# Performance work log

Measured on AMD Instinct MI355X. Metric: run time of the kernel, lower is better.

The kernel has to match this reference:

```python
import jax, jax.numpy as jnp
import numpy as np

N = 100000      # total nodes
E = 1600000     # total edges
B = 256         # graphs in batch
D_IN = 64       # node_in_dim
D_EMB = 128     # node_emb_dim
D_G = 128       # graph_emb_dim
L = 3           # gnn_layers
H1, H2 = 32, 8  # decoder MLP hidden dims
EPS_LN = 1e-5


def layernorm(h, g, b):
    mu = jnp.mean(h, -1, keepdims=True)
    var = jnp.mean((h - mu) ** 2, -1, keepdims=True)
    return (h - mu) * jax.lax.rsqrt(var + EPS_LN) * g + b


def setup_inputs() -> dict:
    key = jax.random.key(0)
    ks = jax.random.split(key, 16)
    gi = D_IN + D_EMB  # skip-conn GNN input dim

    def w(k, shape, fan):
        return jax.random.normal(k, shape, jnp.float32) / np.sqrt(fan).astype(np.float32)

    return {
        "x": jax.random.normal(ks[0], (N, D_IN), jnp.float32),
        "edge_index": jax.random.randint(ks[1], (2, E), 0, N),
        "batch_indices": jnp.sort(jax.random.randint(ks[2], (N,), 0, B)),
        "W_in": w(ks[3], (D_IN, D_EMB), D_IN), "b_in": jnp.zeros((D_EMB,), jnp.float32),
        "eps": jnp.zeros((L,), jnp.float32),  # GINConv train_eps init 0
        "mlp_W1": w(ks[4], (L, gi, D_EMB), gi), "mlp_b1": jnp.zeros((L, D_EMB), jnp.float32),
        "mlp_W2": w(ks[5], (L, D_EMB, D_EMB), D_EMB), "mlp_b2": jnp.zeros((L, D_EMB), jnp.float32),
        "ln_g": jnp.ones((L, D_EMB), jnp.float32), "ln_b": jnp.zeros((L, D_EMB), jnp.float32),
        "out_W": w(ks[6], (D_EMB, D_EMB), D_EMB), "out_b": jnp.zeros((D_EMB,), jnp.float32),
        "lnf_g": jnp.ones((D_EMB,), jnp.float32), "lnf_b": jnp.zeros((D_EMB,), jnp.float32),
        "graph_W": w(ks[7], (D_EMB, D_G), D_EMB), "graph_b": jnp.zeros((D_G,), jnp.float32),
        "gln_g": jnp.ones((D_G,), jnp.float32), "gln_b": jnp.zeros((D_G,), jnp.float32),
        "dW1": w(ks[8], (D_IN + D_EMB, H1), D_IN + D_EMB), "db1": jnp.zeros((H1,), jnp.float32),
        "dW2": w(ks[9], (H1, H2), H1), "db2": jnp.zeros((H2,), jnp.float32),
        "dW3": w(ks[10], (H2, 1), H2), "db3": jnp.zeros((1,), jnp.float32),
        "gW1": w(ks[11], (D_G, H1), D_G), "gb1": jnp.zeros((H1,), jnp.float32),
        "gW2": w(ks[12], (H1, H2), H1), "gb2": jnp.zeros((H2,), jnp.float32),
        "gW3": w(ks[13], (H2, 1), H2), "gb3": jnp.zeros((1,), jnp.float32),
    }


def reference(x, edge_index, batch_indices, W_in, b_in, eps, mlp_W1, mlp_b1, mlp_W2, mlp_b2,
              ln_g, ln_b, out_W, out_b, lnf_g, lnf_b, graph_W, graph_b, gln_g, gln_b,
              dW1, db1, dW2, db2, dW3, db3, gW1, gb1, gW2, gb2, gW3, gb3):
    src, dst = edge_index[0], edge_index[1]
    # Encoder: node_in_fc
    h = jax.nn.relu(x @ W_in + b_in)
    for l in range(L):
        gin = jnp.concatenate([x, h], -1)  # skip_conn: [N, D_IN+D_EMB]
        # GIN message passing: sum-aggregate neighbor features at target nodes
        agg = jax.ops.segment_sum(gin[src], dst, num_segments=N)
        z = (1.0 + eps[l]) * gin + agg
        z = jax.nn.relu(z @ mlp_W1[l] + mlp_b1[l]) @ mlp_W2[l] + mlp_b2[l]
        h = jax.nn.elu(layernorm(z, ln_g[l], ln_b[l]))
    # graph embedding: per-node fc+LN then global mean pool over batch segments
    ge = layernorm(jax.nn.relu(h @ graph_W + graph_b), gln_g, gln_b)
    sums = jax.ops.segment_sum(ge, batch_indices, num_segments=B)
    cnt = jax.ops.segment_sum(jnp.ones((N,), ge.dtype), batch_indices, num_segments=B)
    graph_emb = sums / jnp.maximum(cnt, 1.0)[:, None]
    # node_out_fc + final LN
    node_emb = layernorm(jax.nn.relu(h @ out_W + out_b), lnf_g, lnf_b)
    # Decoder: nodewise MLP on [x, node_emb] (skip_conn)
    ni = jnp.concatenate([x, node_emb], -1)
    no = jax.nn.relu(ni @ dW1 + db1)
    no = (jax.nn.relu(no @ dW2 + db2) @ dW3 + db3)[:, 0]  # [N]
    # graphwise residual MLP
    go = jax.nn.relu(graph_emb @ gW1 + gb1)
    go = (jax.nn.relu(go @ gW2 + gb2) @ gW3 + gb3)[:, 0]  # [B]
    return jnp.concatenate([no, go], -1)  # [N+B]
```

## Files before the change

kernel.cpp:

```cpp
#include <hip/hip_runtime.h>
#include <hip/hip_bf16.h>

#define D_IN 64
#define D_EMB 128
#define GI 192
#define H1 32
#define H2 8

typedef __attribute__((ext_vector_type(8))) short bf16x8;
typedef __attribute__((ext_vector_type(4))) float f32x4;

__device__ __forceinline__ unsigned short f2bf(float f) {
    unsigned int u = __float_as_uint(f);
    return (unsigned short)((u + 0x7fffu + ((u >> 16) & 1u)) >> 16);
}
__device__ __forceinline__ float bflo(unsigned int u) { return __uint_as_float(u << 16); }
__device__ __forceinline__ float bfhi(unsigned int u) { return __uint_as_float(u & 0xffff0000u); }
__device__ __forceinline__ unsigned int pk2(unsigned short a, unsigned short b) {
    return (unsigned int)a | ((unsigned int)b << 16);
}

__global__ __launch_bounds__(256) void hist_part_k(const int* __restrict__ dst, int* __restrict__ cnt,
                                                   int E, int N8) {
    int p = blockIdx.x & 7;
    int base = (blockIdx.x >> 3) * 1024;
    int lo = p * N8, hi = lo + N8;
    #pragma unroll
    for (int t = 0; t < 4; ++t) {
        int e = base + t * 256 + threadIdx.x;
        if (e < E) {
            int d = dst[e];
            if (d >= lo && d < hi) atomicAdd(&cnt[d], 1);
        }
    }
}

__global__ __launch_bounds__(256) void scan1_k(const int* __restrict__ cnt, int* __restrict__ loc,
                                               int* __restrict__ bsum, int N) {
    __shared__ int s[256];
    int tid = threadIdx.x;
    int i = blockIdx.x * 256 + tid;
    int v = (i < N) ? cnt[i] : 0;
    s[tid] = v;
    __syncthreads();
    #pragma unroll
    for (int off = 1; off < 256; off <<= 1) {
        int u = (tid >= off) ? s[tid - off] : 0;
        __syncthreads();
        s[tid] += u;
        __syncthreads();
    }
    int incl = s[tid];
    if (i < N) loc[i] = incl - v;
    if (tid == 255) bsum[blockIdx.x] = incl;
}

__global__ __launch_bounds__(512) void scan2_k(int* __restrict__ bsum, int NB) {
    __shared__ int s[512];
    int tid = threadIdx.x;
    int v = (tid < NB) ? bsum[tid] : 0;
    s[tid] = v;
    __syncthreads();
    #pragma unroll
    for (int off = 1; off < 512; off <<= 1) {
        int u = (tid >= off) ? s[tid - off] : 0;
        __syncthreads();
        s[tid] += u;
        __syncthreads();
    }
    if (tid < NB) bsum[tid] = s[tid] - v;
}

__global__ __launch_bounds__(256) void scan3_k(int* __restrict__ rp, const int* __restrict__ bsum,
                                               int* __restrict__ cursor, int N, int E) {
    int i = blockIdx.x * 256 + threadIdx.x;
    if (i < N) {
        int r = rp[i] + bsum[i >> 8];
        rp[i] = r;
        cursor[i] = r;
    } else if (i == N) {
        rp[N] = E;
    }
}

__global__ __launch_bounds__(256) void scatter_part_k(const int* __restrict__ src, const int* __restrict__ dst,
                                                      int* __restrict__ cursor, int* __restrict__ csr,
                                                      int E, int N8) {
    int p = blockIdx.x & 7;
    int base = (blockIdx.x >> 3) * 1024;
    int lo = p * N8, hi = lo + N8;
    #pragma unroll
    for (int t = 0; t < 4; ++t) {
        int e = base + t * 256 + threadIdx.x;
        if (e < E) {
            int d = dst[e];
            if (d >= lo && d < hi) {
                int s = src[e];
                int pos = atomicAdd(&cursor[d], 1);
                csr[pos] = s;
            }
        }
    }
}

__global__ __launch_bounds__(256) void xcvt_k(const float* __restrict__ x, unsigned short* __restrict__ xb,
                                              int total4) {
    int i = blockIdx.x * 256 + threadIdx.x;
    if (i < total4) {
        float4 v = ((const float4*)x)[i];
        ((uint2*)xb)[i] = make_uint2(pk2(f2bf(v.x), f2bf(v.y)), pk2(f2bf(v.z), f2bf(v.w)));
    }
}

__global__ __launch_bounds__(256) void wfrag_all_k(
    const float* __restrict__ W_in, const float* __restrict__ mlp_W1, const float* __restrict__ mlp_W2,
    const float* __restrict__ graph_W, const float* __restrict__ out_W,
    unsigned short* __restrict__ wf_in, unsigned short* __restrict__ wf_w1,
    unsigned short* __restrict__ wf_w2, unsigned short* __restrict__ wf_graph,
    unsigned short* __restrict__ wf_out) {
    int idx = blockIdx.x * 256 + threadIdx.x;
    const float* src;
    unsigned short* dst;
    int local;
    if (idx < 8192) { src = W_in; dst = wf_in; local = idx; }
    else if (idx < 81920) { int t = idx - 8192; int l = t / 24576; local = t - l * 24576;
                            src = mlp_W1 + (size_t)l * 24576; dst = wf_w1 + (size_t)l * 24576; }
    else if (idx < 131072) { int t = idx - 81920; int l = t / 16384; local = t - l * 16384;
                             src = mlp_W2 + (size_t)l * 16384; dst = wf_w2 + (size_t)l * 16384; }
    else if (idx < 147456) { local = idx - 131072; src = graph_W; dst = wf_graph; }
    else { local = idx - 147456; src = out_W; dst = wf_out; }
    int k = local >> 7, c = local & 127;
    dst[(((size_t)(k >> 3) * 128) + c) * 8 + (k & 7)] = f2bf(src[local]);
}

__global__ __launch_bounds__(256) void agg64b_k(const unsigned short* __restrict__ xb,
                                                const int* __restrict__ rp, const int* __restrict__ cs,
                                                unsigned short* __restrict__ outb, int N) {
    int n = blockIdx.x * 8 + (threadIdx.x >> 5);
    int lane = threadIdx.x & 31;
    if (n >= N) return;
    int bg = rp[n], e = rp[n + 1];
    const unsigned int* x2 = (const unsigned int*)xb;
    float sx = 0.f, sy = 0.f;
    int j = bg;
    for (; j + 3 < e; j += 4) {
        unsigned int v0 = x2[(size_t)cs[j] * 32 + lane];
        unsigned int v1 = x2[(size_t)cs[j + 1] * 32 + lane];
        unsigned int v2 = x2[(size_t)cs[j + 2] * 32 + lane];
        unsigned int v3 = x2[(size_t)cs[j + 3] * 32 + lane];
        sx += bflo(v0) + bflo(v1) + bflo(v2) + bflo(v3);
        sy += bfhi(v0) + bfhi(v1) + bfhi(v2) + bfhi(v3);
    }
    for (; j < e; ++j) {
        unsigned int v = x2[(size_t)cs[j] * 32 + lane];
        sx += bflo(v);
        sy += bfhi(v);
    }
    ((unsigned int*)outb)[(size_t)n * 32 + lane] = pk2(f2bf(sx), f2bf(sy));
}

__global__ __launch_bounds__(256) void zxcvt_k(const unsigned short* __restrict__ xb,
                                               const unsigned short* __restrict__ aggxb,
                                               const float* __restrict__ eps,
                                               unsigned short* __restrict__ zx0,
                                               unsigned short* __restrict__ zx1,
                                               unsigned short* __restrict__ zx2, int total2) {
    int i = blockIdx.x * 256 + threadIdx.x;
    if (i >= total2) return;
    unsigned int xv = ((const unsigned int*)xb)[i];
    unsigned int av = ((const unsigned int*)aggxb)[i];
    float xl = bflo(xv), xh = bfhi(xv), al = bflo(av), ah = bfhi(av);
    float e0 = 1.0f + eps[0], e1 = 1.0f + eps[1], e2 = 1.0f + eps[2];
    ((unsigned int*)zx0)[i] = pk2(f2bf(fmaf(e0, xl, al)), f2bf(fmaf(e0, xh, ah)));
    ((unsigned int*)zx1)[i] = pk2(f2bf(fmaf(e1, xl, al)), f2bf(fmaf(e1, xh, ah)));
    ((unsigned int*)zx2)[i] = pk2(f2bf(fmaf(e2, xl, al)), f2bf(fmaf(e2, xh, ah)));
}

__global__ __launch_bounds__(256) void aggz_k(const unsigned short* __restrict__ hb,
                                              const int* __restrict__ rp, const int* __restrict__ cs,
                                              const float* __restrict__ epsp,
                                              unsigned short* __restrict__ zh, int N) {
    int w = threadIdx.x >> 6, lane = threadIdx.x & 63;
    int n = blockIdx.x * 4 + w;
    if (n >= N) return;
    float es = 1.0f + epsp[0];
    int bg = rp[n], e = rp[n + 1];
    const unsigned int* h2 = (const unsigned int*)hb;
    float sx = 0.f, sy = 0.f;
    int j = bg;
    for (; j + 3 < e; j += 4) {
        unsigned int v0 = h2[(size_t)cs[j] * 64 + lane];
        unsigned int v1 = h2[(size_t)cs[j + 1] * 64 + lane];
        unsigned int v2 = h2[(size_t)cs[j + 2] * 64 + lane];
        unsigned int v3 = h2[(size_t)cs[j + 3] * 64 + lane];
        sx += bflo(v0) + bflo(v1) + bflo(v2) + bflo(v3);
        sy += bfhi(v0) + bfhi(v1) + bfhi(v2) + bfhi(v3);
    }
    for (; j < e; ++j) {
        unsigned int v = h2[(size_t)cs[j] * 64 + lane];
        sx += bflo(v);
        sy += bfhi(v);
    }
    unsigned int hv = h2[(size_t)n * 64 + lane];
    sx = fmaf(es, bflo(hv), sx);
    sy = fmaf(es, bfhi(hv), sy);
    ((unsigned int*)zh)[(size_t)n * 64 + lane] = pk2(f2bf(sx), f2bf(sy));
}

template <int RELU, int ELU>
__device__ __forceinline__ void ln_epilogue(
    f32x4 (&acc)[4][4], const float* __restrict__ bias,
    const float* __restrict__ g, const float* __restrict__ b,
    unsigned short* __restrict__ out,
    int rowBase, int wr, int wc, int lg, int l15, int wh,
    float* rsum, float* rsq, int N) {
    float bv[4], gv[4], bbv[4];
    #pragma unroll
    for (int cb = 0; cb < 4; ++cb) {
        int col = wc + cb * 16 + l15;
        bv[cb] = bias[col];
        gv[cb] = g[col];
        bbv[cb] = b[col];
    }
    float ps[4][4], pq[4][4];
    #pragma unroll
    for (int rb = 0; rb < 4; ++rb)
        #pragma unroll
        for (int q = 0; q < 4; ++q) {
            float s = 0.f, sq = 0.f;
            #pragma unroll
            for (int cb = 0; cb < 4; ++cb) {
                float v = acc[rb][cb][q] + bv[cb];
                if (RELU) v = fmaxf(v, 0.f);
                s += v;
                sq += v * v;
            }
            ps[rb][q] = s;
            pq[rb][q] = sq;
        }
    #pragma unroll
    for (int m = 1; m < 16; m <<= 1) {
        #pragma unroll
        for (int rb = 0; rb < 4; ++rb)
            #pragma unroll
            for (int q = 0; q < 4; ++q) {
                ps[rb][q] += __shfl_xor(ps[rb][q], m, 64);
                pq[rb][q] += __shfl_xor(pq[rb][q], m, 64);
            }
    }
    if (l15 == 0) {
        #pragma unroll
        for (int rb = 0; rb < 4; ++rb)
            #pragma unroll
            for (int q = 0; q < 4; ++q) {
                int row = wr + rb * 16 + lg * 4 + q;
                rsum[wh * 128 + row] = ps[rb][q];
                rsq[wh * 128 + row] = pq[rb][q];
            }
    }
    __syncthreads();
    #pragma unroll
    for (int rb = 0; rb < 4; ++rb)
        #pragma unroll
        for (int q = 0; q < 4; ++q) {
            int row = wr + rb * 16 + lg * 4 + q;
            float st = rsum[row] + rsum[128 + row];
            float sqt = rsq[row] + rsq[128 + row];
            float mu = st * (1.f / 128.f);
            float var = sqt * (1.f / 128.f) - mu * mu;
            float rs = rsqrtf(var + 1e-5f);
            int grow = rowBase + row;
            if (grow < N) {
                #pragma unroll
                for (int cb = 0; cb < 4; ++cb) {
                    float v = acc[rb][cb][q] + bv[cb];
                    if (RELU) v = fmaxf(v, 0.f);
                    float y = (v - mu) * rs * gv[cb] + bbv[cb];
                    if (ELU) y = y > 0.f ? y : expm1f(y);
                    out[(size_t)grow * D_EMB + wc + cb * 16 + l15] = f2bf(y);
                }
            }
        }
}

__global__ __launch_bounds__(256) void enc_gemm_k(
    const unsigned short* __restrict__ Abf, const unsigned short* __restrict__ Wf,
    const float* __restrict__ bias, unsigned short* __restrict__ C, int N) {
    const int tid = threadIdx.x;
    const int wid = tid >> 6, lane = tid & 63;
    const int l15 = lane & 15, lg = lane >> 4;
    const int rowBase = blockIdx.x * 128;
    const int wr = (wid >> 1) * 64, wc = (wid & 1) * 64;
    f32x4 zero = {0.f, 0.f, 0.f, 0.f};
    f32x4 acc[4][4];
    #pragma unroll
    for (int i = 0; i < 4; ++i)
        #pragma unroll
        for (int j = 0; j < 4; ++j) acc[i][j] = zero;
    const unsigned short* ap[4];
    #pragma unroll
    for (int rb = 0; rb < 4; ++rb)
        ap[rb] = Abf + (size_t)min(rowBase + wr + rb * 16 + l15, N - 1) * D_IN;

    for (int k0 = 0; k0 < D_IN; k0 += 32) {
        const int G = (k0 >> 3) + lg;
        bf16x8 bfr[4];
        #pragma unroll
        for (int cb = 0; cb < 4; ++cb)
            bfr[cb] = *(const bf16x8*)&Wf[(((size_t)G * 128) + wc + cb * 16 + l15) * 8];
        #pragma unroll
        for (int rb = 0; rb < 4; ++rb) {
            bf16x8 afr = *(const bf16x8*)(ap[rb] + G * 8);
            #pragma unroll
            for (int cb = 0; cb < 4; ++cb)
                acc[rb][cb] = __builtin_amdgcn_mfma_f32_16x16x32_bf16(afr, bfr[cb], acc[rb][cb], 0, 0, 0);
        }
    }
    #pragma unroll
    for (int cb = 0; cb < 4; ++cb) {
        int col = wc + cb * 16 + l15;
        float bvv = bias[col];
        #pragma unroll
        for (int rb = 0; rb < 4; ++rb)
            #pragma unroll
            for (int q = 0; q < 4; ++q) {
                int row = rowBase + wr + rb * 16 + lg * 4 + q;
                if (row < N) C[(size_t)row * D_EMB + col] = f2bf(fmaxf(acc[rb][cb][q] + bvv, 0.f));
            }
    }
}

__global__ __launch_bounds__(256) void gin_layer_k(
    const unsigned short* __restrict__ zxl, const unsigned short* __restrict__ zhb,
    const unsigned short* __restrict__ W1f, const float* __restrict__ b1,
    const unsigned short* __restrict__ W2f, const float* __restrict__ b2,
    const float* __restrict__ lng, const float* __restrict__ lnb,
    unsigned short* __restrict__ hbo, int N) {
    __shared__ unsigned short T1[8 * 128 * 8];
    __shared__ float rsum[2 * 128];
    __shared__ float rsq[2 * 128];

    const int tid = threadIdx.x;
    const int wid = tid >> 6, lane = tid & 63;
    const int l15 = lane & 15, lg = lane >> 4;
    const int rowBase = blockIdx.x * 128;
    const int wr = (wid >> 1) * 64, wc = (wid & 1) * 64;
    const int wh = wid & 1;

    f32x4 zero = {0.f, 0.f, 0.f, 0.f};
    f32x4 acc[4][4];
    #pragma unroll
    for (int i = 0; i < 4; ++i)
        #pragma unroll
        for (int j = 0; j < 4; ++j) acc[i][j] = zero;

    const unsigned short* axp[4];
    const unsigned short* ahp[4];
    #pragma unroll
    for (int rb = 0; rb < 4; ++rb) {
        int ar = min(rowBase + wr + rb * 16 + l15, N - 1);
        axp[rb] = zxl + (size_t)ar * D_IN;
        ahp[rb] = zhb + (size_t)ar * D_EMB;
    }

    for (int k0 = 0; k0 < D_IN; k0 += 32) {
        const int G = (k0 >> 3) + lg;
        bf16x8 bfr[4];
        #pragma unroll
        for (int cb = 0; cb < 4; ++cb)
            bfr[cb] = *(const bf16x8*)&W1f[(((size_t)G * 128) + wc + cb * 16 + l15) * 8];
        #pragma unroll
        for (int rb = 0; rb < 4; ++rb) {
            bf16x8 afr = *(const bf16x8*)(axp[rb] + G * 8);
            #pragma unroll
            for (int cb = 0; cb < 4; ++cb)
                acc[rb][cb] = __builtin_amdgcn_mfma_f32_16x16x32_bf16(afr, bfr[cb], acc[rb][cb], 0, 0, 0);
        }
    }
    for (int k0 = D_IN; k0 < GI; k0 += 32) {
        const int G = (k0 >> 3) + lg;
        const int ZG = ((k0 - D_IN) >> 3) + lg;
        bf16x8 bfr[4];
        #pragma unroll
        for (int cb = 0; cb < 4; ++cb)
            bfr[cb] = *(const bf16x8*)&W1f[(((size_t)G * 128) + wc + cb * 16 + l15) * 8];
        #pragma unroll
        for (int rb = 0; rb < 4; ++rb) {
            bf16x8 afr = *(const bf16x8*)(ahp[rb] + ZG * 8);
            #pragma unroll
            for (int cb = 0; cb < 4; ++cb)
                acc[rb][cb] = __builtin_amdgcn_mfma_f32_16x16x32_bf16(afr, bfr[cb], acc[rb][cb], 0, 0, 0);
        }
    }

    f32x4 acc2[4][4];
    #pragma unroll
    for (int i = 0; i < 4; ++i)
        #pragma unroll
        for (int j = 0; j < 4; ++j) acc2[i][j] = zero;

    #pragma unroll
    for (int c = 0; c < 2; ++c) {
        if (c) __syncthreads();
        if (wc == c * 64) {
            #pragma unroll
            for (int cb = 0; cb < 4; ++cb) {
                int col = wc + cb * 16 + l15;
                int tcol = col - c * 64;
                float bvv = b1[col];
                #pragma unroll
                for (int rb = 0; rb < 4; ++rb)
                    #pragma unroll
                    for (int q = 0; q < 4; ++q) {
                        int row = wr + rb * 16 + lg * 4 + q;
                        float v = fmaxf(acc[rb][cb][q] + bvv, 0.f);
                        T1[(((size_t)(tcol >> 3) * 128) + row) * 8 + (tcol & 7)] = f2bf(v);
                    }
            }
        }
        __syncthreads();
        for (int k0 = c * 64; k0 < c * 64 + 64; k0 += 32) {
            const int G = (k0 >> 3) + lg;
            const int TG = G - c * 8;
            bf16x8 bfr[4];
            #pragma unroll
            for (int cb = 0; cb < 4; ++cb)
                bfr[cb] = *(const bf16x8*)&W2f[(((size_t)G * 128) + wc + cb * 16 + l15) * 8];
            #pragma unroll
            for (int rb = 0; rb < 4; ++rb) {
                bf16x8 afr = *(const bf16x8*)&T1[(((size_t)TG * 128) + wr + rb * 16 + l15) * 8];
                #pragma unroll
                for (int cb = 0; cb < 4; ++cb)
                    acc2[rb][cb] = __builtin_amdgcn_mfma_f32_16x16x32_bf16(afr, bfr[cb], acc2[rb][cb], 0, 0, 0);
            }
        }
    }

    ln_epilogue<0, 1>(acc2, b2, lng, lnb, hbo, rowBase, wr, wc, lg, l15, wh, rsum, rsq, N);
}

__global__ __launch_bounds__(256) void fc2_k(
    const unsigned short* __restrict__ Abf,
    const unsigned short* __restrict__ WfG, const float* __restrict__ biasG,
    const float* __restrict__ gG, const float* __restrict__ bG, unsigned short* __restrict__ outG,
    const unsigned short* __restrict__ WfN, const float* __restrict__ biasN,
    const float* __restrict__ gN, const float* __restrict__ bN, unsigned short* __restrict__ outN,
    int N) {
    __shared__ float rsum[2 * 128];
    __shared__ float rsq[2 * 128];
    const int tid = threadIdx.x;
    const int wid = tid >> 6, lane = tid & 63;
    const int l15 = lane & 15, lg = lane >> 4;
    const int rowBase = blockIdx.x * 128;
    const int wr = (wid >> 1) * 64, wc = (wid & 1) * 64;
    const int wh = wid & 1;
    f32x4 zero = {0.f, 0.f, 0.f, 0.f};
    f32x4 accG[4][4], accN[4][4];
    #pragma unroll
    for (int i = 0; i < 4; ++i)
        #pragma unroll
        for (int j = 0; j < 4; ++j) { accG[i][j] = zero; accN[i][j] = zero; }
    const unsigned short* ap[4];
    #pragma unroll
    for (int rb = 0; rb < 4; ++rb)
        ap[rb] = Abf + (size_t)min(rowBase + wr + rb * 16 + l15, N - 1) * D_EMB;

    for (int k0 = 0; k0 < D_EMB; k0 += 32) {
        const int G = (k0 >> 3) + lg;
        bf16x8 bfrG[4], bfrN[4];
        #pragma unroll
        for (int cb = 0; cb < 4; ++cb) {
            bfrG[cb] = *(const bf16x8*)&WfG[(((size_t)G * 128) + wc + cb * 16 + l15) * 8];
            bfrN[cb] = *(const bf16x8*)&WfN[(((size_t)G * 128) + wc + cb * 16 + l15) * 8];
        }
        #pragma unroll
        for (int rb = 0; rb < 4; ++rb) {
            bf16x8 afr = *(const bf16x8*)(ap[rb] + G * 8);
            #pragma unroll
            for (int cb = 0; cb < 4; ++cb) {
                accG[rb][cb] = __builtin_amdgcn_mfma_f32_16x16x32_bf16(afr, bfrG[cb], accG[rb][cb], 0, 0, 0);
                accN[rb][cb] = __builtin_amdgcn_mfma_f32_16x16x32_bf16(afr, bfrN[cb], accN[rb][cb], 0, 0, 0);
            }
        }
    }
    ln_epilogue<1, 0>(accG, biasG, gG, bG, outG, rowBase, wr, wc, lg, l15, wh, rsum, rsq, N);
    __syncthreads();
    ln_epilogue<1, 0>(accN, biasN, gN, bN, outN, rowBase, wr, wc, lg, l15, wh, rsum, rsq, N);
}

__global__ __launch_bounds__(256) void bounds_k(const int* __restrict__ batch, int* __restrict__ bounds,
                                                int N, int B) {
    int i = blockIdx.x * 256 + threadIdx.x;
    if (i <= B) {
        int lo = 0, hi = N;
        while (lo < hi) { int m = (lo + hi) >> 1; if (batch[m] < i) lo = m + 1; else hi = m; }
        bounds[i] = lo;
    }
}

__global__ __launch_bounds__(128) void pool_part_k(const unsigned short* __restrict__ ge,
                                                   const int* __restrict__ bounds,
                                                   float* __restrict__ gemb) {
    int b = blockIdx.x >> 3;
    int s = blockIdx.x & 7;
    int start = bounds[b], end = bounds[b + 1];
    int len = end - start;
    int c0 = start + (int)(((long long)len * s) >> 3);
    int c1 = start + (int)(((long long)len * (s + 1)) >> 3);
    if (c1 <= c0) return;
    int col = threadIdx.x;
    float sum = 0.f;
    for (int n = c0; n < c1; ++n)
        sum += __uint_as_float((unsigned int)ge[(size_t)n * D_EMB + col] << 16);
    atomicAdd(&gemb[(size_t)b * D_EMB + col], sum);
}

__global__ __launch_bounds__(256) void node_dec_k(
    const float* __restrict__ x, const unsigned short* __restrict__ ne,
    const float* __restrict__ W1, const float* __restrict__ b1,
    const float* __restrict__ W2, const float* __restrict__ b2,
    const float* __restrict__ W3, const float* __restrict__ b3,
    float* __restrict__ out, int N) {
    __shared__ float W1s[GI * H1];
    __shared__ float W2s[H1 * H2];
    __shared__ float W3s[H2];
    __shared__ float b1s[H1], b2s[H2];
    for (int i = threadIdx.x; i < GI * H1; i += 256) W1s[i] = W1[i];
    if (threadIdx.x < H1 * H2) W2s[threadIdx.x] = W2[threadIdx.x];
    if (threadIdx.x < H2) { W3s[threadIdx.x] = W3[threadIdx.x]; b2s[threadIdx.x] = b2[threadIdx.x]; }
    if (threadIdx.x < H1) b1s[threadIdx.x] = b1[threadIdx.x];
    __syncthreads();
    int n = blockIdx.x * 256 + threadIdx.x;
    if (n >= N) return;
    float acc[H1];
    #pragma unroll
    for (int j = 0; j < H1; ++j) acc[j] = b1s[j];
    const float4* xr = (const float4*)(x + (size_t)n * D_IN);
    #pragma unroll 4
    for (int q = 0; q < D_IN / 4; ++q) {
        float4 v = xr[q];
        int k = q * 4;
        #pragma unroll
        for (int j = 0; j < H1; ++j) acc[j] = fmaf(v.x, W1s[(k + 0) * H1 + j], acc[j]);
        #pragma unroll
        for (int j = 0; j < H1; ++j) acc[j] = fmaf(v.y, W1s[(k + 1) * H1 + j], acc[j]);
        #pragma unroll
        for (int j = 0; j < H1; ++j) acc[j] = fmaf(v.z, W1s[(k + 2) * H1 + j], acc[j]);
        #pragma unroll
        for (int j = 0; j < H1; ++j) acc[j] = fmaf(v.w, W1s[(k + 3) * H1 + j], acc[j]);
    }
    const uint4* nr = (const uint4*)(ne + (size_t)n * D_EMB);
    #pragma unroll 4
    for (int q = 0; q < 16; ++q) {
        uint4 v = nr[q];
        float f[8] = {bflo(v.x), bfhi(v.x), bflo(v.y), bfhi(v.y),
                      bflo(v.z), bfhi(v.z), bflo(v.w), bfhi(v.w)};
        int k = D_IN + q * 8;
        #pragma unroll
        for (int e = 0; e < 8; ++e) {
            #pragma unroll
            for (int j = 0; j < H1; ++j) acc[j] = fmaf(f[e], W1s[(k + e) * H1 + j], acc[j]);
        }
    }
    #pragma unroll
    for (int j = 0; j < H1; ++j) acc[j] = fmaxf(acc[j], 0.f);
    float a2[H2];
    #pragma unroll
    for (int m = 0; m < H2; ++m) a2[m] = b2s[m];
    #pragma unroll
    for (int j = 0; j < H1; ++j)
        #pragma unroll
        for (int m = 0; m < H2; ++m) a2[m] = fmaf(acc[j], W2s[j * H2 + m], a2[m]);
    float o = b3[0];
    #pragma unroll
    for (int m = 0; m < H2; ++m) o = fmaf(fmaxf(a2[m], 0.f), W3s[m], o);
    out[n] = o;
}

__global__ __launch_bounds__(256) void graph_dec_k(
    const float* __restrict__ gemb, const int* __restrict__ bounds,
    const float* __restrict__ W1, const float* __restrict__ b1,
    const float* __restrict__ W2, const float* __restrict__ b2,
    const float* __restrict__ W3, const float* __restrict__ b3,
    float* __restrict__ out, int B) {
    __shared__ float W1s[D_EMB * H1];
    __shared__ float W2s[H1 * H2];
    __shared__ float W3s[H2];
    __shared__ float b1s[H1], b2s[H2];
    for (int i = threadIdx.x; i < D_EMB * H1; i += 256) W1s[i] = W1[i];
    if (threadIdx.x < H1 * H2) W2s[threadIdx.x] = W2[threadIdx.x];
    if (threadIdx.x < H2) { W3s[threadIdx.x] = W3[threadIdx.x]; b2s[threadIdx.x] = b2[threadIdx.x]; }
    if (threadIdx.x < H1) b1s[threadIdx.x] = b1[threadIdx.x];
    __syncthreads();
    int gidx = threadIdx.x;
    if (gidx >= B) return;
    int len = bounds[gidx + 1] - bounds[gidx];
    float inv = 1.f / fmaxf((float)len, 1.f);
    float acc[H1];
    #pragma unroll
    for (int j = 0; j < H1; ++j) acc[j] = b1s[j];
    const float4* gr = (const float4*)(gemb + (size_t)gidx * D_EMB);
    for (int q = 0; q < D_EMB / 4; ++q) {
        float4 v = gr[q];
        v.x *= inv; v.y *= inv; v.z *= inv; v.w *= inv;
        int k = q * 4;
        #pragma unroll
        for (int j = 0; j < H1; ++j) acc[j] = fmaf(v.x, W1s[(k + 0) * H1 + j], acc[j]);
        #pragma unroll
        for (int j = 0; j < H1; ++j) acc[j] = fmaf(v.y, W1s[(k + 1) * H1 + j], acc[j]);
        #pragma unroll
        for (int j = 0; j < H1; ++j) acc[j] = fmaf(v.z, W1s[(k + 2) * H1 + j], acc[j]);
        #pragma unroll
        for (int j = 0; j < H1; ++j) acc[j] = fmaf(v.w, W1s[(k + 3) * H1 + j], acc[j]);
    }
    #pragma unroll
    for (int j = 0; j < H1; ++j) acc[j] = fmaxf(acc[j], 0.f);
    float a2[H2];
    #pragma unroll
    for (int m = 0; m < H2; ++m) a2[m] = b2s[m];
    #pragma unroll
    for (int j = 0; j < H1; ++j)
        #pragma unroll
        for (int m = 0; m < H2; ++m) a2[m] = fmaf(acc[j], W2s[j * H2 + m], a2[m]);
    float o = b3[0];
    #pragma unroll
    for (int m = 0; m < H2; ++m) o = fmaf(fmaxf(a2[m], 0.f), W3s[m], o);
    out[gidx] = o;
}

extern "C" void kernel_launch(void* const* d_in, const int* in_sizes, int n_in,
                              void* d_out, int out_size, void* d_ws, size_t ws_size,
                              hipStream_t stream) {
    const float* x       = (const float*)d_in[0];
    const int*   ei      = (const int*)d_in[1];
    const int*   batch   = (const int*)d_in[2];
    const float* W_in    = (const float*)d_in[3];
    const float* b_in    = (const float*)d_in[4];
    const float* eps     = (const float*)d_in[5];
    const float* mlp_W1  = (const float*)d_in[6];
    const float* mlp_b1  = (const float*)d_in[7];
    const float* mlp_W2  = (const float*)d_in[8];
    const float* mlp_b2  = (const float*)d_in[9];
    const float* ln_g    = (const float*)d_in[10];
    const float* ln_b    = (const float*)d_in[11];
    const float* out_W   = (const float*)d_in[12];
    const float* out_b   = (const float*)d_in[13];
    const float* lnf_g   = (const float*)d_in[14];
    const float* lnf_b   = (const float*)d_in[15];
    const float* graph_W = (const float*)d_in[16];
    const float* graph_b = (const float*)d_in[17];
    const float* gln_g   = (const float*)d_in[18];
    const float* gln_b   = (const float*)d_in[19];
    const float* dW1     = (const float*)d_in[20];
    const float* db1     = (const float*)d_in[21];
    const float* dW2     = (const float*)d_in[22];
    const float* db2     = (const float*)d_in[23];
    const float* dW3     = (const float*)d_in[24];
    const float* db3     = (const float*)d_in[25];
    const float* gW1     = (const float*)d_in[26];
    const float* gb1     = (const float*)d_in[27];
    const float* gW2     = (const float*)d_in[28];
    const float* gb2     = (const float*)d_in[29];
    const float* gW3     = (const float*)d_in[30];
    const float* gb3     = (const float*)d_in[31];
    float* out = (float*)d_out;

    const int N = in_sizes[0] / D_IN;
    const int E = in_sizes[1] / 2;
    const int B = out_size - N;
    const int N8 = (N + 7) / 8;

    const int* esrc = ei;
    const int* edst = ei + E;

    size_t off = 0;
    auto alloc = [&](size_t bytes) { size_t o = off; off += (bytes + 255) & ~(size_t)255; return o; };
    char* ws = (char*)d_ws;
    unsigned short* xb    = (unsigned short*)(ws + alloc((size_t)N * D_IN * 2));
    unsigned short* hb0   = (unsigned short*)(ws + alloc((size_t)N * D_EMB * 2));
    unsigned short* hb1   = (unsigned short*)(ws + alloc((size_t)N * D_EMB * 2));
    unsigned short* zh    = (unsigned short*)(ws + alloc((size_t)N * D_EMB * 2));
    unsigned short* aggxb = (unsigned short*)(ws + alloc((size_t)N * D_IN * 2));
    unsigned short* zx0   = (unsigned short*)(ws + alloc((size_t)N * D_IN * 2));
    unsigned short* zx1   = (unsigned short*)(ws + alloc((size_t)N * D_IN * 2));
    unsigned short* zx2   = (unsigned short*)(ws + alloc((size_t)N * D_IN * 2));
    float* gemb = (float*)(ws + alloc((size_t)B * D_EMB * 4));
    unsigned short* wfpool = (unsigned short*)(ws + alloc((size_t)163840 * 2));
    int* row_ptr = (int*)(ws + alloc((size_t)(N + 1) * 4));
    int* cnt     = (int*)(ws + alloc((size_t)N * 4));
    int* bsum    = (int*)(ws + alloc(512 * 4));
    int* bounds  = (int*)(ws + alloc((size_t)(B + 1) * 4));
    int* csr     = (int*)(ws + alloc((size_t)E * 4));
    (void)ws_size;

    unsigned short* wf_in    = wfpool;
    unsigned short* wf_w1    = wf_in + (size_t)64 * 128;
    unsigned short* wf_w2    = wf_w1 + (size_t)3 * 192 * 128;
    unsigned short* wf_graph = wf_w2 + (size_t)3 * 128 * 128;
    unsigned short* wf_out   = wf_graph + (size_t)128 * 128;

    unsigned short* zxs[3] = {zx0, zx1, zx2};

    const int NB = (N + 255) / 256;
    const int gridEP = 8 * ((E + 1023) / 1024);
    const int gridN4 = (N + 3) / 4;
    const int gridG = (N + 127) / 128;

    hipMemsetAsync(cnt, 0, (size_t)N * 4, stream);
    hist_part_k<<<gridEP, 256, 0, stream>>>(edst, cnt, E, N8);
    scan1_k<<<NB, 256, 0, stream>>>(cnt, row_ptr, bsum, N);
    scan2_k<<<1, 512, 0, stream>>>(bsum, NB);
    scan3_k<<<(N + 256) / 256, 256, 0, stream>>>(row_ptr, bsum, cnt, N, E);
    scatter_part_k<<<gridEP, 256, 0, stream>>>(esrc, edst, cnt, csr, E, N8);

    xcvt_k<<<(N * D_IN / 4 + 255) / 256, 256, 0, stream>>>(x, xb, N * D_IN / 4);
    wfrag_all_k<<<640, 256, 0, stream>>>(W_in, mlp_W1, mlp_W2, graph_W, out_W,
                                         wf_in, wf_w1, wf_w2, wf_graph, wf_out);
    bounds_k<<<(B + 256) / 256, 256, 0, stream>>>(batch, bounds, N, B);
    hipMemsetAsync(gemb, 0, (size_t)B * D_EMB * 4, stream);

    agg64b_k<<<(N + 7) / 8, 256, 0, stream>>>(xb, row_ptr, csr, aggxb, N);
    zxcvt_k<<<(N * 32 + 255) / 256, 256, 0, stream>>>(xb, aggxb, eps, zx0, zx1, zx2, N * 32);

    enc_gemm_k<<<gridG, 256, 0, stream>>>(xb, wf_in, b_in, hb0, N);

    unsigned short* hin = hb0;
    unsigned short* hout = hb1;
    for (int l = 0; l < 3; ++l) {
        aggz_k<<<gridN4, 256, 0, stream>>>(hin, row_ptr, csr, eps + l, zh, N);
        gin_layer_k<<<gridG, 256, 0, stream>>>(zxs[l], zh,
                                               wf_w1 + (size_t)l * 192 * 128, mlp_b1 + (size_t)l * D_EMB,
                                               wf_w2 + (size_t)l * 128 * 128, mlp_b2 + (size_t)l * D_EMB,
                                               ln_g + (size_t)l * D_EMB, ln_b + (size_t)l * D_EMB,
                                               hout, N);
        unsigned short* t = hin; hin = hout; hout = t;
    }
    unsigned short* zb  = hb0;
    unsigned short* neb = zh;

    fc2_k<<<gridG, 256, 0, stream>>>(hin,
                                     wf_graph, graph_b, gln_g, gln_b, zb,
                                     wf_out, out_b, lnf_g, lnf_b, neb, N);
    pool_part_k<<<B * 8, 128, 0, stream>>>(zb, bounds, gemb);

    node_dec_k<<<(N + 255) / 256, 256, 0, stream>>>(x, neb, dW1, db1, dW2, db2, dW3, db3, out, N);
    graph_dec_k<<<1, 256, 0, stream>>>(gemb, bounds, gW1, gb1, gW2, gb2, gW3, gb3, out + N, B);
}
```

Before: 931.4 us.

## Stage activation tiles in LDS with coalesced loads across GEMM kernels

The encoder, GIN-layer and output FC kernels now copy each block's 128-row activation tile into shared memory with coalesced 16-byte loads, then read MFMA A-fragments from LDS. Before, each wave re-read strided rows straight from global memory, and two waves shared each row. The GIN layer also writes the full 128-wide hidden tile into the same LDS buffer in one pass. This replaces the old two-phase half-tile staging with a single pass and fewer barriers. The cost is more LDS per block, about 48KB in the GIN kernel, which may lower occupancy, plus an extra barrier before compute.

```diff
diff --git a/kernel.cpp b/kernel.cpp
--- a/kernel.cpp
+++ b/kernel.cpp
@@ -286,21 +286,31 @@
 __global__ __launch_bounds__(256) void enc_gemm_k(
     const unsigned short* __restrict__ Abf, const unsigned short* __restrict__ Wf,
     const float* __restrict__ bias, unsigned short* __restrict__ C, int N) {
+    __shared__ unsigned short AT[8 * 128 * 8];
     const int tid = threadIdx.x;
     const int wid = tid >> 6, lane = tid & 63;
     const int l15 = lane & 15, lg = lane >> 4;
     const int rowBase = blockIdx.x * 128;
     const int wr = (wid >> 1) * 64, wc = (wid & 1) * 64;
+
+    {
+        int row = tid >> 1, half = tid & 1;
+        int ar = min(rowBase + row, N - 1);
+        const uint4* src = (const uint4*)(Abf + (size_t)ar * D_IN + half * 32);
+        #pragma unroll
+        for (int j = 0; j < 4; ++j) {
+            int g = half * 4 + j;
+            *(uint4*)&AT[(((size_t)g * 128) + row) * 8] = src[j];
+        }
+    }
+    __syncthreads();
+
     f32x4 zero = {0.f, 0.f, 0.f, 0.f};
     f32x4 acc[4][4];
     #pragma unroll
     for (int i = 0; i < 4; ++i)
         #pragma unroll
         for (int j = 0; j < 4; ++j) acc[i][j] = zero;
-    const unsigned short* ap[4];
-    #pragma unroll
-    for (int rb = 0; rb < 4; ++rb)
-        ap[rb] = Abf + (size_t)min(rowBase + wr + rb * 16 + l15, N - 1) * D_IN;
 
     for (int k0 = 0; k0 < D_IN; k0 += 32) {
         const int G = (k0 >> 3) + lg;
@@ -310,7 +320,7 @@
             bfr[cb] = *(const bf16x8*)&Wf[(((size_t)G * 128) + wc + cb * 16 + l15) * 8];
         #pragma unroll
         for (int rb = 0; rb < 4; ++rb) {
-            bf16x8 afr = *(const bf16x8*)(ap[rb] + G * 8);
+            bf16x8 afr = *(const bf16x8*)&AT[(((size_t)G * 128) + wr + rb * 16 + l15) * 8];
             #pragma unroll
             for (int cb = 0; cb < 4; ++cb)
                 acc[rb][cb] = __builtin_amdgcn_mfma_f32_16x16x32_bf16(afr, bfr[cb], acc[rb][cb], 0, 0, 0);
@@ -336,7 +346,7 @@
     const unsigned short* __restrict__ W2f, const float* __restrict__ b2,
     const float* __restrict__ lng, const float* __restrict__ lnb,
     unsigned short* __restrict__ hbo, int N) {
-    __shared__ unsigned short T1[8 * 128 * 8];
+    __shared__ unsigned short AT[24 * 128 * 8];
     __shared__ float rsum[2 * 128];
     __shared__ float rsq[2 * 128];
 
@@ -347,6 +357,24 @@
     const int wr = (wid >> 1) * 64, wc = (wid & 1) * 64;
     const int wh = wid & 1;
 
+    {
+        int row = tid >> 1, half = tid & 1;
+        int ar = min(rowBase + row, N - 1);
+        const uint4* sx = (const uint4*)(zxl + (size_t)ar * D_IN + half * 32);
+        #pragma unroll
+        for (int j = 0; j < 4; ++j) {
+            int g = half * 4 + j;
+            *(uint4*)&AT[(((size_t)g * 128) + row) * 8] = sx[j];
+        }
+        const uint4* sh = (const uint4*)(zhb + (size_t)ar * D_EMB + half * 64);
+        #pragma unroll
+        for (int j = 0; j < 8; ++j) {
+            int g = 8 + half * 8 + j;
+            *(uint4*)&AT[(((size_t)g * 128) + row) * 8] = sh[j];
+        }
+    }
+    __syncthreads();
+
     f32x4 zero = {0.f, 0.f, 0.f, 0.f};
     f32x4 acc[4][4];
     #pragma unroll
@@ -354,16 +382,7 @@
         #pragma unroll
         for (int j = 0; j < 4; ++j) acc[i][j] = zero;
 
-    const unsigned short* axp[4];
-    const unsigned short* ahp[4];
-    #pragma unroll
-    for (int rb = 0; rb < 4; ++rb) {
-        int ar = min(rowBase + wr + rb * 16 + l15, N - 1);
-        axp[rb] = zxl + (size_t)ar * D_IN;
-        ahp[rb] = zhb + (size_t)ar * D_EMB;
-    }
-
-    for (int k0 = 0; k0 < D_IN; k0 += 32) {
+    for (int k0 = 0; k0 < GI; k0 += 32) {
         const int G = (k0 >> 3) + lg;
         bf16x8 bfr[4];
         #pragma unroll
@@ -371,68 +390,46 @@
             bfr[cb] = *(const bf16x8*)&W1f[(((size_t)G * 128) + wc + cb * 16 + l15) * 8];
         #pragma unroll
         for (int rb = 0; rb < 4; ++rb) {
-            bf16x8 afr = *(const bf16x8*)(axp[rb] + G * 8);
+            bf16x8 afr = *(const bf16x8*)&AT[(((size_t)G * 128) + wr + rb * 16 + l15) * 8];
             #pragma unroll
             for (int cb = 0; cb < 4; ++cb)
                 acc[rb][cb] = __builtin_amdgcn_mfma_f32_16x16x32_bf16(afr, bfr[cb], acc[rb][cb], 0, 0, 0);
         }
     }
-    for (int k0 = D_IN; k0 < GI; k0 += 32) {
+
+    __syncthreads();
+    #pragma unroll
+    for (int cb = 0; cb < 4; ++cb) {
+        int col = wc + cb * 16 + l15;
+        float bvv = b1[col];
+        #pragma unroll
+        for (int rb = 0; rb < 4; ++rb)
+            #pragma unroll
+            for (int q = 0; q < 4; ++q) {
+                int row = wr + rb * 16 + lg * 4 + q;
+                float v = fmaxf(acc[rb][cb][q] + bvv, 0.f);
+                AT[(((size_t)(col >> 3) * 128) + row) * 8 + (col & 7)] = f2bf(v);
+            }
+    }
+    __syncthreads();
+
+    f32x4 acc2[4][4];
+    #pragma unroll
+    for (int i = 0; i < 4; ++i)
+        #pragma unroll
+        for (int j = 0; j < 4; ++j) acc2[i][j] = zero;
+    for (int k0 = 0; k0 < D_EMB; k0 += 32) {
         const int G = (k0 >> 3) + lg;
-        const int ZG = ((k0 - D_IN) >> 3) + lg;
         bf16x8 bfr[4];
         #pragma unroll
         for (int cb = 0; cb < 4; ++cb)
-            bfr[cb] = *(const bf16x8*)&W1f[(((size_t)G * 128) + wc + cb * 16 + l15) * 8];
+            bfr[cb] = *(const bf16x8*)&W2f[(((size_t)G * 128) + wc + cb * 16 + l15) * 8];
         #pragma unroll
         for (int rb = 0; rb < 4; ++rb) {
-            bf16x8 afr = *(const bf16x8*)(ahp[rb] + ZG * 8);
+            bf16x8 afr = *(const bf16x8*)&AT[(((size_t)G * 128) + wr + rb * 16 + l15) * 8];
             #pragma unroll
             for (int cb = 0; cb < 4; ++cb)
-                acc[rb][cb] = __builtin_amdgcn_mfma_f32_16x16x32_bf16(afr, bfr[cb], acc[rb][cb], 0, 0, 0);
-        }
-    }
-
-    f32x4 acc2[4][4];
-    #pragma unroll
-    for (int i = 0; i < 4; ++i)
-        #pragma unroll
-        for (int j = 0; j < 4; ++j) acc2[i][j] = zero;
-
-    #pragma unroll
-    for (int c = 0; c < 2; ++c) {
-        if (c) __syncthreads();
-        if (wc == c * 64) {
-            #pragma unroll
-            for (int cb = 0; cb < 4; ++cb) {
-                int col = wc + cb * 16 + l15;
-                int tcol = col - c * 64;
-                float bvv = b1[col];
-                #pragma unroll
-                for (int rb = 0; rb < 4; ++rb)
-                    #pragma unroll
-                    for (int q = 0; q < 4; ++q) {
-                        int row = wr + rb * 16 + lg * 4 + q;
-                        float v = fmaxf(acc[rb][cb][q] + bvv, 0.f);
-                        T1[(((size_t)(tcol >> 3) * 128) + row) * 8 + (tcol & 7)] = f2bf(v);
-                    }
-            }
-        }
-        __syncthreads();
-        for (int k0 = c * 64; k0 < c * 64 + 64; k0 += 32) {
-            const int G = (k0 >> 3) + lg;
-            const int TG = G - c * 8;
-            bf16x8 bfr[4];
-            #pragma unroll
-            for (int cb = 0; cb < 4; ++cb)
-                bfr[cb] = *(const bf16x8*)&W2f[(((size_t)G * 128) + wc + cb * 16 + l15) * 8];
-            #pragma unroll
-            for (int rb = 0; rb < 4; ++rb) {
-                bf16x8 afr = *(const bf16x8*)&T1[(((size_t)TG * 128) + wr + rb * 16 + l15) * 8];
-                #pragma unroll
-                for (int cb = 0; cb < 4; ++cb)
-                    acc2[rb][cb] = __builtin_amdgcn_mfma_f32_16x16x32_bf16(afr, bfr[cb], acc2[rb][cb], 0, 0, 0);
-            }
+                acc2[rb][cb] = __builtin_amdgcn_mfma_f32_16x16x32_bf16(afr, bfr[cb], acc2[rb][cb], 0, 0, 0);
         }
     }
 
@@ -446,6 +443,7 @@
     const unsigned short* __restrict__ WfN, const float* __restrict__ biasN,
     const float* __restrict__ gN, const float* __restrict__ bN, unsigned short* __restrict__ outN,
     int N) {
+    __shared__ unsigned short AT[16 * 128 * 8];
     __shared__ float rsum[2 * 128];
     __shared__ float rsq[2 * 128];
     const int tid = threadIdx.x;
@@ -454,16 +452,25 @@
     const int rowBase = blockIdx.x * 128;
     const int wr = (wid >> 1) * 64, wc = (wid & 1) * 64;
     const int wh = wid & 1;
+
+    {
+        int row = tid >> 1, half = tid & 1;
+        int ar = min(rowBase + row, N - 1);
+        const uint4* src = (const uint4*)(Abf + (size_t)ar * D_EMB + half * 64);
+        #pragma unroll
+        for (int j = 0; j < 8; ++j) {
+            int g = half * 8 + j;
+            *(uint4*)&AT[(((size_t)g * 128) + row) * 8] = src[j];
+        }
+    }
+    __syncthreads();
+
     f32x4 zero = {0.f, 0.f, 0.f, 0.f};
     f32x4 accG[4][4], accN[4][4];
     #pragma unroll
     for (int i = 0; i < 4; ++i)
         #pragma unroll
         for (int j = 0; j < 4; ++j) { accG[i][j] = zero; accN[i][j] = zero; }
-    const unsigned short* ap[4];
-    #pragma unroll
-    for (int rb = 0; rb < 4; ++rb)
-        ap[rb] = Abf + (size_t)min(rowBase + wr + rb * 16 + l15, N - 1) * D_EMB;
 
     for (int k0 = 0; k0 < D_EMB; k0 += 32) {
         const int G = (k0 >> 3) + lg;
@@ -475,7 +482,7 @@
         }
         #pragma unroll
         for (int rb = 0; rb < 4; ++rb) {
-            bf16x8 afr = *(const bf16x8*)(ap[rb] + G * 8);
+            bf16x8 afr = *(const bf16x8*)&AT[(((size_t)G * 128) + wr + rb * 16 + l15) * 8];
             #pragma unroll
             for (int cb = 0; cb < 4; ++cb) {
                 accG[rb][cb] = __builtin_amdgcn_mfma_f32_16x16x32_bf16(afr, bfrG[cb], accG[rb][cb], 0, 0, 0);
```

Measured after the change: 828.3 us. -11.1%, faster.
